# Kernel optimization log

Measured on AMD Instinct MI355X. Metric: run time of the kernel, lower is better.

## Reference

```python
import jax, jax.numpy as jnp
import numpy as np

B, GH, GW = 64, 14, 14
H = 512   # features_len == lstm hidden size == lstm_len
E = 512   # embedding_len
A = 512   # attention_len
V = 10000 # wordmap_len
MAXCAP = 50


def setup_inputs() -> dict:
    key = jax.random.key(0)
    ks = jax.random.split(key, 12)
    s = 0.02
    caplens = jax.random.randint(ks[2], (B, 1), 2, MAXCAP + 1, jnp.int32)
    caplens = caplens.at[0, 0].set(MAXCAP)  # ensure max(decode_lengths) == MAXCAP-1 (static T)
    return dict(
        image_features=jax.random.normal(ks[0], (B, GH, GW, H), jnp.float32),
        caps=jax.random.randint(ks[1], (B, MAXCAP), 0, V, jnp.int32),
        caplens=caplens,
        emb_table=jax.random.normal(ks[3], (V, E), jnp.float32) * s,
        W_ih=jax.random.normal(ks[4], (4 * H, E + H), jnp.float32) * s,
        W_hh=jax.random.normal(ks[5], (4 * H, H), jnp.float32) * s,
        b_ih=jnp.zeros((4 * H,), jnp.float32),
        b_hh=jnp.zeros((4 * H,), jnp.float32),
        W_enc=jax.random.normal(ks[6], (A, H), jnp.float32) * s,
        b_enc=jnp.zeros((A,), jnp.float32),
        W_dec=jax.random.normal(ks[7], (A, H), jnp.float32) * s,
        b_dec=jnp.zeros((A,), jnp.float32),
        W_full=jax.random.normal(ks[8], (1, A), jnp.float32) * s,
        b_full=jnp.zeros((1,), jnp.float32),
        W_score=jax.random.normal(ks[9], (V, H), jnp.float32) * s,
        b_score=jnp.zeros((V,), jnp.float32),
    )


def _forward(image_features, emb_table, W_ih, W_hh, b_ih, b_hh,
             W_enc, b_enc, W_dec, b_dec, W_full, b_full, W_score, b_score,
             caps, caplens):
    Bsz = image_features.shape[0]
    feats = image_features.reshape(Bsz, -1, image_features.shape[-1])  # (B, P, H)
    cl = caplens[:, 0]
    sort_ind = jnp.argsort(-cl)                      # descending sort by caption length
    cl = cl[sort_ind]
    feats = feats[sort_ind]
    caps_s = caps[sort_ind]
    decode_lengths = cl - 1
    T = caps.shape[1] - 1                            # static; setup guarantees max(decode_lengths)==T
    emb = emb_table[caps_s]                          # (B, MAXCAP, E)
    enc_att = jnp.einsum('bph,ah->bpa', feats, W_enc) + b_enc  # precomputed encoder attention proj
    mask = jnp.arange(T)[None, :] < decode_lengths[:, None]    # (B, T): row active at step t

    h0 = jnp.zeros((Bsz, feats.shape[-1]), feats.dtype)
    c0 = jnp.zeros_like(h0)

    def step(carry, xs):
        h, c = carry
        emb_t, m_t = xs                              # (B,E), (B,)
        # attention (show-attend-tell style)
        att2 = h @ W_dec.T + b_dec                   # (B, A)
        e = jnp.einsum('bpa,a->bp', jax.nn.relu(enc_att + att2[:, None, :]), W_full[0]) + b_full[0]
        alpha = jax.nn.softmax(e, axis=-1)           # (B, P)
        ctx = jnp.einsum('bp,bph->bh', alpha, feats) # (B, H)
        # LSTMCell
        x = jnp.concatenate([emb_t, ctx], axis=1)    # (B, E+H)
        gates = x @ W_ih.T + b_ih + h @ W_hh.T + b_hh
        i, f, g, o = jnp.split(gates, 4, axis=1)
        c_new = jax.nn.sigmoid(f) * c + jax.nn.sigmoid(i) * jnp.tanh(g)
        h_new = jax.nn.sigmoid(o) * jnp.tanh(c_new)
        score = h_new @ W_score.T + b_score          # (B, V)
        m = m_t[:, None]
        # rows past their decode length keep stale state and write zeros (matches :k slicing)
        h = jnp.where(m, h_new, h)
        c = jnp.where(m, c_new, c)
        return (h, c), (jnp.where(m, score, jnp.zeros((), score.dtype)),
                        jnp.where(m, alpha, jnp.zeros((), alpha.dtype)))

    (_, _), (scores, weights) = jax.lax.scan(
        step, (h0, c0), (emb[:, :T, :].transpose(1, 0, 2), mask.T))
    scores = scores.transpose(1, 0, 2)   # (B, T, V)
    weights = weights.transpose(1, 0, 2) # (B, T, P)
    return scores, caps_s, decode_lengths, weights, sort_ind


def reference(image_features, caps, caplens, emb_table, W_ih, W_hh, b_ih, b_hh,
              W_enc, b_enc, W_dec, b_dec, W_full, b_full, W_score, b_score):
    return _forward(image_features, emb_table, W_ih, W_hh, b_ih, b_hh,
                    W_enc, b_enc, W_dec, b_dec, W_full, b_full, W_score, b_score,
                    caps, caplens)
```

## Files before the change

### kernel.cpp

```cpp
#include <hip/hip_runtime.h>
#include <math.h>


#define WS_SORT   0
#define WS_DL     64
#define WS_NB     128
#define WS_ROWOFF 192
#define WS_CAPS   256
#define WS_RMAP   3456
#define WS_H      6592
#define WS_C      39360
#define WS_ATT2   72128
#define WS_E      104896
#define WS_Z      117696
#define WS_CTXP   117952
#define WS_PG     249024
#define WS_HALL   2346176
#define WS_ENC    3951808

#define OUT_SCORES 0
#define OUT_CAPS   31360000
#define OUT_DL     31363200
#define OUT_W      31363264
#define OUT_SORT   31977920

#define KC  32
#define LST 68

__device__ __forceinline__ float sigm(float x) { return 1.f / (1.f + expf(-x)); }

__device__ __forceinline__ void gemm_acc(const float* __restrict__ As, const float* __restrict__ Bs,
                                         float acc[8][8], int tx, int ty) {
#pragma unroll 8
  for (int kk = 0; kk < KC; ++kk) {
    const float4* ar = (const float4*)(As + kk * LST + tx * 8);
    const float4* br = (const float4*)(Bs + kk * LST + ty * 8);
    float4 a0 = ar[0], a1 = ar[1];
    float4 b0 = br[0], b1 = br[1];
    float av[8] = {a0.x, a0.y, a0.z, a0.w, a1.x, a1.y, a1.z, a1.w};
    float bv[8] = {b0.x, b0.y, b0.z, b0.w, b1.x, b1.y, b1.z, b1.w};
#pragma unroll
    for (int i = 0; i < 8; ++i)
#pragma unroll
      for (int j = 0; j < 8; ++j)
        acc[i][j] = fmaf(av[i], bv[j], acc[i][j]);
  }
}

__device__ __forceinline__ void load_tile_strided(const float* __restrict__ src, int row0, int ld, int k0,
                                                  float* __restrict__ dst, int tid, int nrows_valid) {
#pragma unroll
  for (int i = 0; i < 8; ++i) {
    int lin = tid + 64 * i;
    int m = lin >> 3, kf = lin & 7;
    float4 v = make_float4(0.f, 0.f, 0.f, 0.f);
    if (m < nrows_valid) v = *(const float4*)(src + (long)(row0 + m) * ld + k0 + kf * 4);
    dst[(kf * 4 + 0) * LST + m] = v.x;
    dst[(kf * 4 + 1) * LST + m] = v.y;
    dst[(kf * 4 + 2) * LST + m] = v.z;
    dst[(kf * 4 + 3) * LST + m] = v.w;
  }
}

__device__ __forceinline__ void load_tile_gather(const float* __restrict__ src, const int* __restrict__ bases,
                                                 int k0, float* __restrict__ dst, int tid) {
#pragma unroll
  for (int i = 0; i < 8; ++i) {
    int lin = tid + 64 * i;
    int m = lin >> 3, kf = lin & 7;
    float4 v = *(const float4*)(src + bases[m] + k0 + kf * 4);
    dst[(kf * 4 + 0) * LST + m] = v.x;
    dst[(kf * 4 + 1) * LST + m] = v.y;
    dst[(kf * 4 + 2) * LST + m] = v.z;
    dst[(kf * 4 + 3) * LST + m] = v.w;
  }
}

__global__ __launch_bounds__(64) void setup_kernel(const int* __restrict__ caps, const int* __restrict__ caplens,
                                                   float* __restrict__ ws, float* __restrict__ out) {
  __shared__ int cl_s[64], so_s[64], dl_s[64], nb_s[49], ro_s[50];
  int i = threadIdx.x;
  cl_s[i] = caplens[i];
  __syncthreads();
  int cli = cl_s[i];
  int r = 0;
  for (int j = 0; j < 64; ++j) {
    int clj = cl_s[j];
    r += (clj > cli) || (clj == cli && j < i);
  }
  so_s[r] = i;
  dl_s[r] = cli - 1;
  __syncthreads();
  int* iws = (int*)ws;
  iws[WS_SORT + i] = so_s[i];
  iws[WS_DL + i] = dl_s[i];
  out[OUT_SORT + i] = (float)so_s[i];
  out[OUT_DL + i] = (float)dl_s[i];
  if (i < 49) {
    int n = 0;
    for (int b = 0; b < 64; ++b) n += (dl_s[b] > i);
    iws[WS_NB + i] = n;
    nb_s[i] = n;
  }
  __syncthreads();
  if (i == 0) {
    int acc = 0;
    for (int t = 0; t < 49; ++t) { ro_s[t] = acc; acc += nb_s[t]; }
    ro_s[49] = acc;
    iws[WS_NB + 49] = acc;
  }
  __syncthreads();
  if (i < 50) iws[WS_ROWOFF + i] = ro_s[i];
  int R = ro_s[49];
  for (int rr = i; rr < 3136; rr += 64) {
    int val = 0;
    if (rr < R) {
      int t = 0;
      while (t < 48 && ro_s[t + 1] <= rr) ++t;
      val = t * 64 + (rr - ro_s[t]);
    }
    iws[WS_RMAP + rr] = val;
  }
  for (int j = i; j < 3200; j += 64) {
    int k = j / 50, jj = j - k * 50;
    int cv = caps[so_s[k] * 50 + jj];
    iws[WS_CAPS + j] = cv;
    out[OUT_CAPS + j] = (float)cv;
  }
}

__global__ void zero_init_kernel(float* __restrict__ out, float* __restrict__ ws, const float* __restrict__ b_dec) {
  const float4 z = make_float4(0.f, 0.f, 0.f, 0.f);
  float4* out4 = (float4*)out;
  float4* ws4 = (float4*)ws;
  const float4* bd4 = (const float4*)b_dec;
  for (long idx = (long)blockIdx.x * 256 + threadIdx.x; idx < 8018240L; idx += (long)gridDim.x * 256) {
    if (idx < 7840000L) {
      out4[idx] = z;
    } else if (idx < 7993664L) {
      out4[7840816L + (idx - 7840000L)] = z;
    } else if (idx < 8010048L) {
      ws4[1648L + (idx - 7993664L)] = z;
    } else {
      long j = idx - 8010048L;
      ws4[18032L + j] = bd4[j & 127];
    }
  }
}

__global__ __launch_bounds__(64) void encatt_kernel(const float* __restrict__ image, const float* __restrict__ W_enc,
                                                    const float* __restrict__ b_enc, float* __restrict__ ws) {
  __shared__ __align__(16) float As[KC * LST];
  __shared__ __align__(16) float Bs[KC * LST];
  __shared__ int rb[64];
  int tid = threadIdx.x;
  const int* iws = (const int*)ws;
  int mt = blockIdx.x, nt = blockIdx.y;
  {
    int r = mt * 64 + tid;
    int b = r / 196;
    int p = r - b * 196;
    rb[tid] = iws[WS_SORT + b] * 100352 + p * 512;
  }
  float acc[8][8] = {};
  for (int ch = 0; ch < 16; ++ch) {
    __syncthreads();
    load_tile_gather(image, rb, ch * 32, As, tid);
    load_tile_strided(W_enc, nt * 64, 512, ch * 32, Bs, tid, 64);
    __syncthreads();
    gemm_acc(As, Bs, acc, tid & 7, tid >> 3);
  }
  int tx = tid & 7, ty = tid >> 3;
  int r0 = mt * 64 + tx * 8;
  int n0 = nt * 64 + ty * 8;
#pragma unroll
  for (int i = 0; i < 8; ++i) {
    float* cp = ws + WS_ENC + (long)(r0 + i) * 512 + n0;
    *(float4*)(cp)     = make_float4(acc[i][0] + b_enc[n0],     acc[i][1] + b_enc[n0 + 1],
                                     acc[i][2] + b_enc[n0 + 2], acc[i][3] + b_enc[n0 + 3]);
    *(float4*)(cp + 4) = make_float4(acc[i][4] + b_enc[n0 + 4], acc[i][5] + b_enc[n0 + 5],
                                     acc[i][6] + b_enc[n0 + 6], acc[i][7] + b_enc[n0 + 7]);
  }
}

__global__ __launch_bounds__(256) void ectx_kernel(float* __restrict__ ws, const float* __restrict__ image,
                                                   const float* __restrict__ W_full, const float* __restrict__ b_full,
                                                   int t) {
  const int* iws = (const int*)ws;
  int b = blockIdx.x;
  if (b >= iws[WS_NB + t]) return;
  int pg = blockIdx.y;
  __shared__ float att2_s[512], wf_s[512], e_s[52];
  int tid = threadIdx.x;
  for (int a = tid; a < 512; a += 256) {
    att2_s[a] = ws[WS_ATT2 + b * 512 + a];
    wf_s[a] = W_full[a];
  }
  __syncthreads();
  int w = tid >> 6, lane = tid & 63;
  float bf0 = b_full[0];
  for (int idx = w; idx < 49; idx += 4) {
    int p = pg * 49 + idx;
    const float* er = ws + WS_ENC + (long)(b * 196 + p) * 512;
    float acc = 0.f;
#pragma unroll
    for (int a8 = 0; a8 < 8; ++a8) {
      int a = (a8 << 6) + lane;
      float v = er[a] + att2_s[a];
      acc = fmaf(fmaxf(v, 0.f), wf_s[a], acc);
    }
#pragma unroll
    for (int off = 32; off; off >>= 1) acc += __shfl_down(acc, off);
    if (lane == 0) e_s[idx] = expf(acc + bf0);
  }
  __syncthreads();
  if (tid < 49) ws[WS_E + b * 200 + pg * 49 + tid] = e_s[tid];
  if (tid == 0) {
    float zz = 0.f;
    for (int j = 0; j < 49; ++j) zz += e_s[j];
    ws[WS_Z + pg * 64 + b] = zz;
  }
  long sb = (long)iws[WS_SORT + b] * 100352;
  float a0 = 0.f, a1 = 0.f;
  for (int j = 0; j < 49; ++j) {
    float al = e_s[j];
    const float* fp = image + sb + (long)(pg * 49 + j) * 512;
    a0 = fmaf(al, fp[tid], a0);
    a1 = fmaf(al, fp[tid + 256], a1);
  }
  ws[WS_CTXP + pg * 32768 + b * 512 + tid] = a0;
  ws[WS_CTXP + pg * 32768 + b * 512 + 256 + tid] = a1;
}

__global__ __launch_bounds__(64) void gates_kernel(float* __restrict__ ws, const float* __restrict__ emb,
                                                   const float* __restrict__ W_ih, const float* __restrict__ W_hh,
                                                   int t) {
  __shared__ __align__(16) float As[KC * LST];
  __shared__ __align__(16) float Bs[KC * LST];
  __shared__ int rbe[64];
  __shared__ float rcpz_s[64];
  int tid = threadIdx.x;
  int nt = blockIdx.x;
  int ks = blockIdx.y;
  int* iws = (int*)ws;
  rbe[tid] = iws[WS_CAPS + tid * 50 + t] * 512;
  {
    float zz = ws[WS_Z + tid] + ws[WS_Z + 64 + tid] + ws[WS_Z + 128 + tid] + ws[WS_Z + 192 + tid];
    rcpz_s[tid] = 1.f / zz;
  }
  float acc[8][8] = {};
  for (int ch = 0; ch < 3; ++ch) {
    int k0 = ks * 96 + ch * 32;
    __syncthreads();
    if (k0 < 512) {
      load_tile_gather(emb, rbe, k0, As, tid);
    } else if (k0 < 1024) {
      int kc = k0 - 512;
#pragma unroll
      for (int i = 0; i < 8; ++i) {
        int lin = tid + 64 * i;
        int m = lin >> 3, kf = lin & 7;
        const float* base = ws + WS_CTXP + m * 512 + kc + kf * 4;
        float4 v0 = *(const float4*)(base);
        float4 v1 = *(const float4*)(base + 32768);
        float4 v2 = *(const float4*)(base + 65536);
        float4 v3 = *(const float4*)(base + 98304);
        float rz = rcpz_s[m];
        As[(kf * 4 + 0) * LST + m] = (v0.x + v1.x + v2.x + v3.x) * rz;
        As[(kf * 4 + 1) * LST + m] = (v0.y + v1.y + v2.y + v3.y) * rz;
        As[(kf * 4 + 2) * LST + m] = (v0.z + v1.z + v2.z + v3.z) * rz;
        As[(kf * 4 + 3) * LST + m] = (v0.w + v1.w + v2.w + v3.w) * rz;
      }
    } else {
      load_tile_strided(ws + WS_H, 0, 512, k0 - 1024, As, tid, 64);
    }
    if (k0 < 1024) load_tile_strided(W_ih, nt * 64, 1024, k0, Bs, tid, 64);
    else           load_tile_strided(W_hh, nt * 64, 512, k0 - 1024, Bs, tid, 64);
    __syncthreads();
    gemm_acc(As, Bs, acc, tid & 7, tid >> 3);
  }
  int tx = tid & 7, ty = tid >> 3;
  float* pg = ws + WS_PG + ks * 131072;
  int j0 = nt * 64 + ty * 8;
#pragma unroll
  for (int i = 0; i < 8; ++i) {
    int b = tx * 8 + i;
    float* cp = pg + b * 2048 + j0;
    *(float4*)(cp)     = make_float4(acc[i][0], acc[i][1], acc[i][2], acc[i][3]);
    *(float4*)(cp + 4) = make_float4(acc[i][4], acc[i][5], acc[i][6], acc[i][7]);
  }
}

__global__ __launch_bounds__(512) void lstm_att2_kernel(float* __restrict__ ws, const float* __restrict__ b_ih,
                                                        const float* __restrict__ b_hh, const float* __restrict__ W_dec,
                                                        const float* __restrict__ b_dec, float* __restrict__ out, int t) {
  const int* iws = (const int*)ws;
  int b = blockIdx.x;
  int as = blockIdx.y;
  int hh = threadIdx.x;
  int nb = iws[WS_NB + t];
  __shared__ float h_s[512], red[512];
  float gi = b_ih[hh] + b_hh[hh];
  float gf = b_ih[512 + hh] + b_hh[512 + hh];
  float gg = b_ih[1024 + hh] + b_hh[1024 + hh];
  float go = b_ih[1536 + hh] + b_hh[1536 + hh];
  const float* pgp = ws + WS_PG + b * 2048;
#pragma unroll
  for (int ks = 0; ks < 16; ++ks) {
    const float* p = pgp + ks * 131072;
    gi += p[hh]; gf += p[512 + hh]; gg += p[1024 + hh]; go += p[1536 + hh];
  }
  float c = ws[WS_C + b * 512 + hh];
  float cn = sigm(gf) * c + sigm(gi) * tanhf(gg);
  float hn = sigm(go) * tanhf(cn);
  h_s[hh] = hn;
  if (b < nb) {
    if (as == 0) {
      ws[WS_C + b * 512 + hh] = cn;
      ws[WS_H + b * 512 + hh] = hn;
      ws[WS_HALL + (long)(iws[WS_ROWOFF + t] + b) * 512 + hh] = hn;
    }
    if (hh < 49) {
      float zz = ws[WS_Z + b] + ws[WS_Z + 64 + b] + ws[WS_Z + 128 + b] + ws[WS_Z + 192 + b];
      int p = as * 49 + hh;
      out[OUT_W + (long)(b * 49 + t) * 196 + p] = ws[WS_E + b * 200 + p] / zz;
    }
  }
  __syncthreads();
  int a = as * 128 + (hh >> 2);
  int part = hh & 3;
  const float* wd = W_dec + (long)a * 512 + part * 128;
  const float* hp = h_s + part * 128;
  float s = 0.f;
#pragma unroll 8
  for (int j = 0; j < 32; ++j) {
    float4 wv = *(const float4*)(wd + 4 * j);
    s = fmaf(hp[4 * j], wv.x, s);
    s = fmaf(hp[4 * j + 1], wv.y, s);
    s = fmaf(hp[4 * j + 2], wv.z, s);
    s = fmaf(hp[4 * j + 3], wv.w, s);
  }
  red[hh] = s;
  __syncthreads();
  if (part == 0) {
    float v = red[hh] + red[hh + 1] + red[hh + 2] + red[hh + 3] + b_dec[a];
    ws[WS_ATT2 + b * 512 + a] = v;
  }
}

__global__ __launch_bounds__(64) void score_kernel(const float* __restrict__ ws, const float* __restrict__ W_score,
                                                   const float* __restrict__ b_score, float* __restrict__ out) {
  __shared__ __align__(16) float As[KC * LST];
  __shared__ __align__(16) float Bs[KC * LST];
  const int* iws = (const int*)ws;
  int mt = blockIdx.x, nt = blockIdx.y;
  int R = iws[WS_NB + 49];
  if (mt * 64 >= R) return;
  int tid = threadIdx.x;
  int mvalid = R - mt * 64; if (mvalid > 64) mvalid = 64;
  int nvalid = 10000 - nt * 64; if (nvalid > 64) nvalid = 64;
  float acc[8][8] = {};
  for (int ch = 0; ch < 16; ++ch) {
    __syncthreads();
    load_tile_strided(ws + WS_HALL, mt * 64, 512, ch * 32, As, tid, mvalid);
    load_tile_strided(W_score, nt * 64, 512, ch * 32, Bs, tid, nvalid);
    __syncthreads();
    gemm_acc(As, Bs, acc, tid & 7, tid >> 3);
  }
  int tx = tid & 7, ty = tid >> 3;
  int n0 = nt * 64 + ty * 8;
#pragma unroll
  for (int i = 0; i < 8; ++i) {
    int r = mt * 64 + tx * 8 + i;
    if (r >= R) continue;
    int tb = iws[WS_RMAP + r];
    int bb = tb & 63, tt = tb >> 6;
    float* cp = out + (long)bb * 490000 + tt * 10000 + n0;
    if (n0 + 4 <= 10000)
      *(float4*)(cp)     = make_float4(acc[i][0] + b_score[n0],     acc[i][1] + b_score[n0 + 1],
                                       acc[i][2] + b_score[n0 + 2], acc[i][3] + b_score[n0 + 3]);
    if (n0 + 8 <= 10000)
      *(float4*)(cp + 4) = make_float4(acc[i][4] + b_score[n0 + 4], acc[i][5] + b_score[n0 + 5],
                                       acc[i][6] + b_score[n0 + 6], acc[i][7] + b_score[n0 + 7]);
  }
}

extern "C" void kernel_launch(void* const* d_in, const int* in_sizes, int n_in,
                              void* d_out, int out_size, void* d_ws, size_t ws_size,
                              hipStream_t stream) {
  const float* image   = (const float*)d_in[0];
  const int*   caps    = (const int*)d_in[1];
  const int*   caplens = (const int*)d_in[2];
  const float* emb     = (const float*)d_in[3];
  const float* W_ih    = (const float*)d_in[4];
  const float* W_hh    = (const float*)d_in[5];
  const float* b_ih    = (const float*)d_in[6];
  const float* b_hh    = (const float*)d_in[7];
  const float* W_enc   = (const float*)d_in[8];
  const float* b_enc   = (const float*)d_in[9];
  const float* W_dec   = (const float*)d_in[10];
  const float* b_dec   = (const float*)d_in[11];
  const float* W_full  = (const float*)d_in[12];
  const float* b_full  = (const float*)d_in[13];
  const float* W_score = (const float*)d_in[14];
  const float* b_score = (const float*)d_in[15];
  float* out = (float*)d_out;
  float* ws  = (float*)d_ws;

  setup_kernel<<<1, 64, 0, stream>>>(caps, caplens, ws, out);
  zero_init_kernel<<<2048, 256, 0, stream>>>(out, ws, b_dec);
  encatt_kernel<<<dim3(196, 8), 64, 0, stream>>>(image, W_enc, b_enc, ws);
  for (int t = 0; t < 49; ++t) {
    ectx_kernel<<<dim3(64, 4), 256, 0, stream>>>(ws, image, W_full, b_full, t);
    gates_kernel<<<dim3(32, 16), 64, 0, stream>>>(ws, emb, W_ih, W_hh, t);
    lstm_att2_kernel<<<dim3(64, 4), 512, 0, stream>>>(ws, b_ih, b_hh, W_dec, b_dec, out, t);
  }
  score_kernel<<<dim3(49, 157), 64, 0, stream>>>(ws, W_score, b_score, out);
}
```

Baseline: 2.873 ms.

## Fuse per-step decoder kernels into one persistent kernel with grid barriers

Replaces the 147 per-timestep launches (ectx, gates, lstm_att2) with a single persistent 256-block kernel that loops over all 49 steps and separates phases with an atomic-counter grid barrier. The gates GEMM is remapped so each 256-thread block runs two 64x64 tiles, splitting K across wave pairs and reducing them through shared memory. The LSTM/att2 phase now uses 256 threads with float4 partial-gate sums. This targets launch overhead and inter-kernel gaps, but relies on all 256 blocks being co-resident to avoid deadlock and adds spin-wait barrier latency.

```diff
diff --git a/kernel.cpp b/kernel.cpp
--- a/kernel.cpp
+++ b/kernel.cpp
@@ -17,6 +17,7 @@
 #define WS_PG     249024
 #define WS_HALL   2346176
 #define WS_ENC    3951808
+#define WS_BAR    (WS_NB + 60)
 
 #define OUT_SCORES 0
 #define OUT_CAPS   31360000
@@ -28,6 +29,10 @@
 #define LST 68
 
 __device__ __forceinline__ float sigm(float x) { return 1.f / (1.f + expf(-x)); }
+
+__device__ __forceinline__ float4 f4add(float4 a, float4 b) {
+  return make_float4(a.x + b.x, a.y + b.y, a.z + b.z, a.w + b.w);
+}
 
 __device__ __forceinline__ void gemm_acc(const float* __restrict__ As, const float* __restrict__ Bs,
                                          float acc[8][8], int tx, int ty) {
@@ -76,6 +81,17 @@
   }
 }
 
+__device__ __forceinline__ void gsync(int* bar, int target) {
+  __syncthreads();
+  if (threadIdx.x == 0) {
+    __hip_atomic_fetch_add(bar, 1, __ATOMIC_RELEASE, __HIP_MEMORY_SCOPE_AGENT);
+    while (__hip_atomic_load(bar, __ATOMIC_RELAXED, __HIP_MEMORY_SCOPE_AGENT) < target)
+      __builtin_amdgcn_s_sleep(1);
+    __threadfence();
+  }
+  __syncthreads();
+}
+
 __global__ __launch_bounds__(64) void setup_kernel(const int* __restrict__ caps, const int* __restrict__ caplens,
                                                    float* __restrict__ ws, float* __restrict__ out) {
   __shared__ int cl_s[64], so_s[64], dl_s[64], nb_s[49], ro_s[50];
@@ -92,6 +108,7 @@
   dl_s[r] = cli - 1;
   __syncthreads();
   int* iws = (int*)ws;
+  if (i == 0) iws[WS_BAR] = 0;
   iws[WS_SORT + i] = so_s[i];
   iws[WS_DL + i] = dl_s[i];
   out[OUT_SORT + i] = (float)so_s[i];
@@ -183,168 +200,222 @@
   }
 }
 
-__global__ __launch_bounds__(256) void ectx_kernel(float* __restrict__ ws, const float* __restrict__ image,
-                                                   const float* __restrict__ W_full, const float* __restrict__ b_full,
-                                                   int t) {
+__global__ __launch_bounds__(256) void loop_kernel(
+    float* __restrict__ ws, const float* __restrict__ image, const float* __restrict__ emb,
+    const float* __restrict__ W_ih, const float* __restrict__ W_hh,
+    const float* __restrict__ b_ih, const float* __restrict__ b_hh,
+    const float* __restrict__ W_dec, const float* __restrict__ b_dec,
+    const float* __restrict__ W_full, const float* __restrict__ b_full,
+    float* __restrict__ out) {
+  __shared__ __align__(16) float sm[8704];
+  int* bar = ((int*)ws) + WS_BAR;
   const int* iws = (const int*)ws;
-  int b = blockIdx.x;
-  if (b >= iws[WS_NB + t]) return;
-  int pg = blockIdx.y;
-  __shared__ float att2_s[512], wf_s[512], e_s[52];
+  int blk = blockIdx.x;
   int tid = threadIdx.x;
-  for (int a = tid; a < 512; a += 256) {
-    att2_s[a] = ws[WS_ATT2 + b * 512 + a];
-    wf_s[a] = W_full[a];
-  }
-  __syncthreads();
-  int w = tid >> 6, lane = tid & 63;
-  float bf0 = b_full[0];
-  for (int idx = w; idx < 49; idx += 4) {
-    int p = pg * 49 + idx;
-    const float* er = ws + WS_ENC + (long)(b * 196 + p) * 512;
-    float acc = 0.f;
-#pragma unroll
-    for (int a8 = 0; a8 < 8; ++a8) {
-      int a = (a8 << 6) + lane;
-      float v = er[a] + att2_s[a];
-      acc = fmaf(fmaxf(v, 0.f), wf_s[a], acc);
+  int syncno = 0;
+
+  for (int t = 0; t < 49; ++t) {
+    int nbt = iws[WS_NB + t];
+
+    {
+      int b = blk >> 2, pg = blk & 3;
+      if (b < nbt) {
+        float* att2_s = sm;
+        float* wf_s = sm + 512;
+        float* e_s = sm + 1024;
+        for (int a = tid; a < 512; a += 256) {
+          att2_s[a] = ws[WS_ATT2 + b * 512 + a];
+          wf_s[a] = W_full[a];
+        }
+        __syncthreads();
+        int w = tid >> 6, lane = tid & 63;
+        float bf0 = b_full[0];
+        for (int idx = w; idx < 49; idx += 4) {
+          int p = pg * 49 + idx;
+          const float* er = ws + WS_ENC + (long)(b * 196 + p) * 512;
+          float acc = 0.f;
+#pragma unroll
+          for (int a8 = 0; a8 < 8; ++a8) {
+            int a = (a8 << 6) + lane;
+            float v = er[a] + att2_s[a];
+            acc = fmaf(fmaxf(v, 0.f), wf_s[a], acc);
+          }
+#pragma unroll
+          for (int off = 32; off; off >>= 1) acc += __shfl_down(acc, off);
+          if (lane == 0) e_s[idx] = expf(acc + bf0);
+        }
+        __syncthreads();
+        if (tid < 49) ws[WS_E + b * 200 + pg * 49 + tid] = e_s[tid];
+        if (tid == 0) {
+          float zz = 0.f;
+          for (int j = 0; j < 49; ++j) zz += e_s[j];
+          ws[WS_Z + pg * 64 + b] = zz;
+        }
+        long sb = (long)iws[WS_SORT + b] * 100352;
+        float a0 = 0.f, a1 = 0.f;
+        for (int j = 0; j < 49; ++j) {
+          float al = e_s[j];
+          const float* fp = image + sb + (long)(pg * 49 + j) * 512;
+          a0 = fmaf(al, fp[tid], a0);
+          a1 = fmaf(al, fp[tid + 256], a1);
+        }
+        ws[WS_CTXP + pg * 32768 + b * 512 + tid] = a0;
+        ws[WS_CTXP + pg * 32768 + b * 512 + 256 + tid] = a1;
+      }
     }
-#pragma unroll
-    for (int off = 32; off; off >>= 1) acc += __shfl_down(acc, off);
-    if (lane == 0) e_s[idx] = expf(acc + bf0);
-  }
-  __syncthreads();
-  if (tid < 49) ws[WS_E + b * 200 + pg * 49 + tid] = e_s[tid];
-  if (tid == 0) {
-    float zz = 0.f;
-    for (int j = 0; j < 49; ++j) zz += e_s[j];
-    ws[WS_Z + pg * 64 + b] = zz;
-  }
-  long sb = (long)iws[WS_SORT + b] * 100352;
-  float a0 = 0.f, a1 = 0.f;
-  for (int j = 0; j < 49; ++j) {
-    float al = e_s[j];
-    const float* fp = image + sb + (long)(pg * 49 + j) * 512;
-    a0 = fmaf(al, fp[tid], a0);
-    a1 = fmaf(al, fp[tid + 256], a1);
-  }
-  ws[WS_CTXP + pg * 32768 + b * 512 + tid] = a0;
-  ws[WS_CTXP + pg * 32768 + b * 512 + 256 + tid] = a1;
-}
-
-__global__ __launch_bounds__(64) void gates_kernel(float* __restrict__ ws, const float* __restrict__ emb,
-                                                   const float* __restrict__ W_ih, const float* __restrict__ W_hh,
-                                                   int t) {
-  __shared__ __align__(16) float As[KC * LST];
-  __shared__ __align__(16) float Bs[KC * LST];
-  __shared__ int rbe[64];
-  __shared__ float rcpz_s[64];
-  int tid = threadIdx.x;
-  int nt = blockIdx.x;
-  int ks = blockIdx.y;
-  int* iws = (int*)ws;
-  rbe[tid] = iws[WS_CAPS + tid * 50 + t] * 512;
-  {
-    float zz = ws[WS_Z + tid] + ws[WS_Z + 64 + tid] + ws[WS_Z + 128 + tid] + ws[WS_Z + 192 + tid];
-    rcpz_s[tid] = 1.f / zz;
-  }
-  float acc[8][8] = {};
-  for (int ch = 0; ch < 3; ++ch) {
-    int k0 = ks * 96 + ch * 32;
-    __syncthreads();
-    if (k0 < 512) {
-      load_tile_gather(emb, rbe, k0, As, tid);
-    } else if (k0 < 1024) {
-      int kc = k0 - 512;
-#pragma unroll
-      for (int i = 0; i < 8; ++i) {
-        int lin = tid + 64 * i;
-        int m = lin >> 3, kf = lin & 7;
-        const float* base = ws + WS_CTXP + m * 512 + kc + kf * 4;
-        float4 v0 = *(const float4*)(base);
-        float4 v1 = *(const float4*)(base + 32768);
-        float4 v2 = *(const float4*)(base + 65536);
-        float4 v3 = *(const float4*)(base + 98304);
-        float rz = rcpz_s[m];
-        As[(kf * 4 + 0) * LST + m] = (v0.x + v1.x + v2.x + v3.x) * rz;
-        As[(kf * 4 + 1) * LST + m] = (v0.y + v1.y + v2.y + v3.y) * rz;
-        As[(kf * 4 + 2) * LST + m] = (v0.z + v1.z + v2.z + v3.z) * rz;
-        As[(kf * 4 + 3) * LST + m] = (v0.w + v1.w + v2.w + v3.w) * rz;
-      }
-    } else {
-      load_tile_strided(ws + WS_H, 0, 512, k0 - 1024, As, tid, 64);
+    ++syncno; gsync(bar, 256 * syncno);
+
+    {
+      int w = tid >> 6, lane = tid & 63;
+      int pairIdx = w >> 1, sub = w & 1;
+      int vb = blk * 2 + pairIdx;
+      int nt = vb & 31, ks = vb >> 5;
+      float* As_w = sm + w * 1088;
+      float* Bs_w = sm + 4352 + w * 1088;
+      int tx = lane & 7, ty = lane >> 3;
+      float acc[8][8] = {};
+      for (int c = 0; c < 3; ++c) {
+        int k0 = ks * 96 + (sub * 3 + c) * 16;
+#pragma unroll
+        for (int i = 0; i < 4; ++i) {
+          int lin = lane + 64 * i;
+          int m = lin >> 2, kf = lin & 3;
+          float4 v;
+          if (k0 < 512) {
+            v = *(const float4*)(emb + (long)iws[WS_CAPS + m * 50 + t] * 512 + k0 + kf * 4);
+          } else if (k0 < 1024) {
+            const float* base = ws + WS_CTXP + m * 512 + (k0 - 512) + kf * 4;
+            float4 v0 = *(const float4*)(base);
+            float4 v1 = *(const float4*)(base + 32768);
+            float4 v2 = *(const float4*)(base + 65536);
+            float4 v3 = *(const float4*)(base + 98304);
+            float rz = 1.f / (ws[WS_Z + m] + ws[WS_Z + 64 + m] + ws[WS_Z + 128 + m] + ws[WS_Z + 192 + m]);
+            v = make_float4((v0.x + v1.x + v2.x + v3.x) * rz, (v0.y + v1.y + v2.y + v3.y) * rz,
+                            (v0.z + v1.z + v2.z + v3.z) * rz, (v0.w + v1.w + v2.w + v3.w) * rz);
+          } else {
+            v = *(const float4*)(ws + WS_H + m * 512 + (k0 - 1024) + kf * 4);
+          }
+          As_w[(kf * 4 + 0) * 68 + m] = v.x;
+          As_w[(kf * 4 + 1) * 68 + m] = v.y;
+          As_w[(kf * 4 + 2) * 68 + m] = v.z;
+          As_w[(kf * 4 + 3) * 68 + m] = v.w;
+        }
+#pragma unroll
+        for (int i = 0; i < 4; ++i) {
+          int lin = lane + 64 * i;
+          int m = lin >> 2, kf = lin & 3;
+          const float* src = (k0 < 1024) ? (W_ih + (long)(nt * 64 + m) * 1024 + k0 + kf * 4)
+                                         : (W_hh + (long)(nt * 64 + m) * 512 + (k0 - 1024) + kf * 4);
+          float4 v = *(const float4*)src;
+          Bs_w[(kf * 4 + 0) * 68 + m] = v.x;
+          Bs_w[(kf * 4 + 1) * 68 + m] = v.y;
+          Bs_w[(kf * 4 + 2) * 68 + m] = v.z;
+          Bs_w[(kf * 4 + 3) * 68 + m] = v.w;
+        }
+        __syncthreads();
+#pragma unroll
+        for (int kk = 0; kk < 16; ++kk) {
+          const float4* ar4 = (const float4*)(As_w + kk * 68 + tx * 8);
+          const float4* br4 = (const float4*)(Bs_w + kk * 68 + ty * 8);
+          float4 a0v = ar4[0], a1v = ar4[1];
+          float4 b0v = br4[0], b1v = br4[1];
+          float av[8] = {a0v.x, a0v.y, a0v.z, a0v.w, a1v.x, a1v.y, a1v.z, a1v.w};
+          float bv[8] = {b0v.x, b0v.y, b0v.z, b0v.w, b1v.x, b1v.y, b1v.z, b1v.w};
+#pragma unroll
+          for (int i = 0; i < 8; ++i)
+#pragma unroll
+            for (int j = 0; j < 8; ++j)
+              acc[i][j] = fmaf(av[i], bv[j], acc[i][j]);
+        }
+        __syncthreads();
+      }
+      float* ar = sm + pairIdx * 4096;
+      if (sub == 0) {
+#pragma unroll
+        for (int i = 0; i < 8; ++i) {
+          float* dp = ar + (tx * 8 + i) * 64 + ty * 8;
+          *(float4*)(dp)     = make_float4(acc[i][0], acc[i][1], acc[i][2], acc[i][3]);
+          *(float4*)(dp + 4) = make_float4(acc[i][4], acc[i][5], acc[i][6], acc[i][7]);
+        }
+      }
+      __syncthreads();
+      if (sub == 1) {
+        float* pgout = ws + WS_PG + ks * 131072;
+#pragma unroll
+        for (int i = 0; i < 8; ++i) {
+          const float* sp = ar + (tx * 8 + i) * 64 + ty * 8;
+          float4 r0 = *(const float4*)(sp);
+          float4 r1 = *(const float4*)(sp + 4);
+          float* cp = pgout + (tx * 8 + i) * 2048 + nt * 64 + ty * 8;
+          *(float4*)(cp)     = make_float4(acc[i][0] + r0.x, acc[i][1] + r0.y,
+                                           acc[i][2] + r0.z, acc[i][3] + r0.w);
+          *(float4*)(cp + 4) = make_float4(acc[i][4] + r1.x, acc[i][5] + r1.y,
+                                           acc[i][6] + r1.z, acc[i][7] + r1.w);
+        }
+      }
     }
-    if (k0 < 1024) load_tile_strided(W_ih, nt * 64, 1024, k0, Bs, tid, 64);
-    else           load_tile_strided(W_hh, nt * 64, 512, k0 - 1024, Bs, tid, 64);
-    __syncthreads();
-    gemm_acc(As, Bs, acc, tid & 7, tid >> 3);
-  }
-  int tx = tid & 7, ty = tid >> 3;
-  float* pg = ws + WS_PG + ks * 131072;
-  int j0 = nt * 64 + ty * 8;
-#pragma unroll
-  for (int i = 0; i < 8; ++i) {
-    int b = tx * 8 + i;
-    float* cp = pg + b * 2048 + j0;
-    *(float4*)(cp)     = make_float4(acc[i][0], acc[i][1], acc[i][2], acc[i][3]);
-    *(float4*)(cp + 4) = make_float4(acc[i][4], acc[i][5], acc[i][6], acc[i][7]);
-  }
-}
-
-__global__ __launch_bounds__(512) void lstm_att2_kernel(float* __restrict__ ws, const float* __restrict__ b_ih,
-                                                        const float* __restrict__ b_hh, const float* __restrict__ W_dec,
-                                                        const float* __restrict__ b_dec, float* __restrict__ out, int t) {
-  const int* iws = (const int*)ws;
-  int b = blockIdx.x;
-  int as = blockIdx.y;
-  int hh = threadIdx.x;
-  int nb = iws[WS_NB + t];
-  __shared__ float h_s[512], red[512];
-  float gi = b_ih[hh] + b_hh[hh];
-  float gf = b_ih[512 + hh] + b_hh[512 + hh];
-  float gg = b_ih[1024 + hh] + b_hh[1024 + hh];
-  float go = b_ih[1536 + hh] + b_hh[1536 + hh];
-  const float* pgp = ws + WS_PG + b * 2048;
-#pragma unroll
-  for (int ks = 0; ks < 16; ++ks) {
-    const float* p = pgp + ks * 131072;
-    gi += p[hh]; gf += p[512 + hh]; gg += p[1024 + hh]; go += p[1536 + hh];
-  }
-  float c = ws[WS_C + b * 512 + hh];
-  float cn = sigm(gf) * c + sigm(gi) * tanhf(gg);
-  float hn = sigm(go) * tanhf(cn);
-  h_s[hh] = hn;
-  if (b < nb) {
-    if (as == 0) {
-      ws[WS_C + b * 512 + hh] = cn;
-      ws[WS_H + b * 512 + hh] = hn;
-      ws[WS_HALL + (long)(iws[WS_ROWOFF + t] + b) * 512 + hh] = hn;
+    ++syncno; gsync(bar, 256 * syncno);
+
+    {
+      int b = blk >> 2, as = blk & 3;
+      bool act = (b < nbt);
+      float* g = sm;
+      float* hsh = sm + 2048;
+      float* red = sm + 2560;
+      const float4* bi4 = (const float4*)b_ih;
+      const float4* bh4 = (const float4*)b_hh;
+      const float* pgb = ws + WS_PG + b * 2048;
+      int f0 = tid, f1 = tid + 256;
+      float4 A0 = f4add(bi4[f0], bh4[f0]);
+      float4 A1 = f4add(bi4[f1], bh4[f1]);
+#pragma unroll
+      for (int ksl = 0; ksl < 16; ++ksl) {
+        const float4* p = (const float4*)(pgb + ksl * 131072);
+        A0 = f4add(A0, p[f0]);
+        A1 = f4add(A1, p[f1]);
+      }
+      ((float4*)g)[f0] = A0;
+      ((float4*)g)[f1] = A1;
+      __syncthreads();
+      int ro = iws[WS_ROWOFF + t];
+#pragma unroll
+      for (int r = 0; r < 2; ++r) {
+        int hh = tid + r * 256;
+        float gi = g[hh], gf = g[512 + hh], gg = g[1024 + hh], go = g[1536 + hh];
+        float c = ws[WS_C + b * 512 + hh];
+        float cn = sigm(gf) * c + sigm(gi) * tanhf(gg);
+        float hn = sigm(go) * tanhf(cn);
+        hsh[hh] = hn;
+        if (act && as == 0) {
+          ws[WS_C + b * 512 + hh] = cn;
+          ws[WS_H + b * 512 + hh] = hn;
+          ws[WS_HALL + (long)(ro + b) * 512 + hh] = hn;
+        }
+      }
+      if (act && tid < 49) {
+        float zz = ws[WS_Z + b] + ws[WS_Z + 64 + b] + ws[WS_Z + 128 + b] + ws[WS_Z + 192 + b];
+        int p = as * 49 + tid;
+        out[OUT_W + (long)(b * 49 + t) * 196 + p] = ws[WS_E + b * 200 + p] / zz;
+      }
+      __syncthreads();
+      int a = as * 128 + (tid >> 1);
+      int part = tid & 1;
+      const float4* wd = (const float4*)(W_dec + (long)a * 512 + part * 256);
+      const float4* hp = (const float4*)(hsh + part * 256);
+      float s = 0.f;
+#pragma unroll 8
+      for (int j = 0; j < 64; ++j) {
+        float4 wv = wd[j], hv = hp[j];
+        s = fmaf(wv.x, hv.x, s);
+        s = fmaf(wv.y, hv.y, s);
+        s = fmaf(wv.z, hv.z, s);
+        s = fmaf(wv.w, hv.w, s);
+      }
+      red[tid] = s;
+      __syncthreads();
+      if (part == 0) ws[WS_ATT2 + b * 512 + a] = red[tid] + red[tid + 1] + b_dec[a];
     }
-    if (hh < 49) {
-      float zz = ws[WS_Z + b] + ws[WS_Z + 64 + b] + ws[WS_Z + 128 + b] + ws[WS_Z + 192 + b];
-      int p = as * 49 + hh;
-      out[OUT_W + (long)(b * 49 + t) * 196 + p] = ws[WS_E + b * 200 + p] / zz;
-    }
-  }
-  __syncthreads();
-  int a = as * 128 + (hh >> 2);
-  int part = hh & 3;
-  const float* wd = W_dec + (long)a * 512 + part * 128;
-  const float* hp = h_s + part * 128;
-  float s = 0.f;
-#pragma unroll 8
-  for (int j = 0; j < 32; ++j) {
-    float4 wv = *(const float4*)(wd + 4 * j);
-    s = fmaf(hp[4 * j], wv.x, s);
-    s = fmaf(hp[4 * j + 1], wv.y, s);
-    s = fmaf(hp[4 * j + 2], wv.z, s);
-    s = fmaf(hp[4 * j + 3], wv.w, s);
-  }
-  red[hh] = s;
-  __syncthreads();
-  if (part == 0) {
-    float v = red[hh] + red[hh + 1] + red[hh + 2] + red[hh + 3] + b_dec[a];
-    ws[WS_ATT2 + b * 512 + a] = v;
+    if (t < 48) { ++syncno; gsync(bar, 256 * syncno); }
   }
 }
 
@@ -410,10 +481,7 @@
   setup_kernel<<<1, 64, 0, stream>>>(caps, caplens, ws, out);
   zero_init_kernel<<<2048, 256, 0, stream>>>(out, ws, b_dec);
   encatt_kernel<<<dim3(196, 8), 64, 0, stream>>>(image, W_enc, b_enc, ws);
-  for (int t = 0; t < 49; ++t) {
-    ectx_kernel<<<dim3(64, 4), 256, 0, stream>>>(ws, image, W_full, b_full, t);
-    gates_kernel<<<dim3(32, 16), 64, 0, stream>>>(ws, emb, W_ih, W_hh, t);
-    lstm_att2_kernel<<<dim3(64, 4), 512, 0, stream>>>(ws, b_ih, b_hh, W_dec, b_dec, out, t);
-  }
+  loop_kernel<<<256, 256, 0, stream>>>(ws, image, emb, W_ih, W_hh, b_ih, b_hh,
+                                       W_dec, b_dec, W_full, b_full, out);
   score_kernel<<<dim3(49, 157), 64, 0, stream>>>(ws, W_score, b_score, out);
 }
```

After: 9.591 ms. 3.34x slower.

## Fuse LSTM cell, decoder attention and context into one per-step kernel; enlarge GEMM tiles

Applied to the files above, without the earlier changes.

Merges the per-step attention/context kernel and the LSTM/att2 kernel into a single step_kernel run by one block per batch row. That block computes the LSTM update, att2, attention softmax and the normalized context for the next step. This cuts the per-step launch count from three to two and removes the partial-sum scratch buffers and the reduction inside the gates kernel. In exchange, only 64 blocks do all 196 pixels of attention per step, which reduces parallelism. The encoder-attention and score GEMMs also move to 128x128 tiles with 256 threads.

```diff
diff --git a/kernel.cpp b/kernel.cpp
--- a/kernel.cpp
+++ b/kernel.cpp
@@ -10,13 +10,10 @@
 #define WS_RMAP   3456
 #define WS_H      6592
 #define WS_C      39360
-#define WS_ATT2   72128
-#define WS_E      104896
-#define WS_Z      117696
-#define WS_CTXP   117952
-#define WS_PG     249024
-#define WS_HALL   2346176
-#define WS_ENC    3951808
+#define WS_CTX    72128
+#define WS_PG     104896
+#define WS_HALL   2202048
+#define WS_ENC    3807680
 
 #define OUT_SCORES 0
 #define OUT_CAPS   31360000
@@ -26,8 +23,13 @@
 
 #define KC  32
 #define LST 68
+#define LKW 132
 
 __device__ __forceinline__ float sigm(float x) { return 1.f / (1.f + expf(-x)); }
+
+__device__ __forceinline__ float4 f4add(float4 a, float4 b) {
+  return make_float4(a.x + b.x, a.y + b.y, a.z + b.z, a.w + b.w);
+}
 
 __device__ __forceinline__ void gemm_acc(const float* __restrict__ As, const float* __restrict__ Bs,
                                          float acc[8][8], int tx, int ty) {
@@ -76,6 +78,53 @@
   }
 }
 
+__device__ __forceinline__ void stage128_strided(const float* __restrict__ src, int row0, int ld, int k0,
+                                                 float* __restrict__ dst, int tid, int nrows_valid) {
+#pragma unroll
+  for (int i = 0; i < 2; ++i) {
+    int lin = tid + 256 * i;
+    int m = lin >> 2, kf = lin & 3;
+    float4 v = make_float4(0.f, 0.f, 0.f, 0.f);
+    if (m < nrows_valid) v = *(const float4*)(src + (long)(row0 + m) * ld + k0 + kf * 4);
+    dst[(kf * 4 + 0) * LKW + m] = v.x;
+    dst[(kf * 4 + 1) * LKW + m] = v.y;
+    dst[(kf * 4 + 2) * LKW + m] = v.z;
+    dst[(kf * 4 + 3) * LKW + m] = v.w;
+  }
+}
+
+__device__ __forceinline__ void stage128_gather(const float* __restrict__ src, const int* __restrict__ bases,
+                                                int k0, float* __restrict__ dst, int tid) {
+#pragma unroll
+  for (int i = 0; i < 2; ++i) {
+    int lin = tid + 256 * i;
+    int m = lin >> 2, kf = lin & 3;
+    float4 v = *(const float4*)(src + bases[m] + k0 + kf * 4);
+    dst[(kf * 4 + 0) * LKW + m] = v.x;
+    dst[(kf * 4 + 1) * LKW + m] = v.y;
+    dst[(kf * 4 + 2) * LKW + m] = v.z;
+    dst[(kf * 4 + 3) * LKW + m] = v.w;
+  }
+}
+
+__device__ __forceinline__ void gemm_acc128(const float* __restrict__ As, const float* __restrict__ Bs,
+                                            float acc[8][8], int tx, int ty) {
+#pragma unroll
+  for (int kk = 0; kk < 16; ++kk) {
+    const float4* ar = (const float4*)(As + kk * LKW + tx * 8);
+    const float4* br = (const float4*)(Bs + kk * LKW + ty * 8);
+    float4 a0 = ar[0], a1 = ar[1];
+    float4 b0 = br[0], b1 = br[1];
+    float av[8] = {a0.x, a0.y, a0.z, a0.w, a1.x, a1.y, a1.z, a1.w};
+    float bv[8] = {b0.x, b0.y, b0.z, b0.w, b1.x, b1.y, b1.z, b1.w};
+#pragma unroll
+    for (int i = 0; i < 8; ++i)
+#pragma unroll
+      for (int j = 0; j < 8; ++j)
+        acc[i][j] = fmaf(av[i], bv[j], acc[i][j]);
+  }
+}
+
 __global__ __launch_bounds__(64) void setup_kernel(const int* __restrict__ caps, const int* __restrict__ caplens,
                                                    float* __restrict__ ws, float* __restrict__ out) {
   __shared__ int cl_s[64], so_s[64], dl_s[64], nb_s[49], ro_s[50];
@@ -129,50 +178,46 @@
   }
 }
 
-__global__ void zero_init_kernel(float* __restrict__ out, float* __restrict__ ws, const float* __restrict__ b_dec) {
+__global__ void zero_init_kernel(float* __restrict__ out, float* __restrict__ ws) {
   const float4 z = make_float4(0.f, 0.f, 0.f, 0.f);
   float4* out4 = (float4*)out;
   float4* ws4 = (float4*)ws;
-  const float4* bd4 = (const float4*)b_dec;
-  for (long idx = (long)blockIdx.x * 256 + threadIdx.x; idx < 8018240L; idx += (long)gridDim.x * 256) {
+  for (long idx = (long)blockIdx.x * 256 + threadIdx.x; idx < 8010048L; idx += (long)gridDim.x * 256) {
     if (idx < 7840000L) {
       out4[idx] = z;
     } else if (idx < 7993664L) {
       out4[7840816L + (idx - 7840000L)] = z;
-    } else if (idx < 8010048L) {
+    } else {
       ws4[1648L + (idx - 7993664L)] = z;
-    } else {
-      long j = idx - 8010048L;
-      ws4[18032L + j] = bd4[j & 127];
-    }
-  }
-}
-
-__global__ __launch_bounds__(64) void encatt_kernel(const float* __restrict__ image, const float* __restrict__ W_enc,
-                                                    const float* __restrict__ b_enc, float* __restrict__ ws) {
-  __shared__ __align__(16) float As[KC * LST];
-  __shared__ __align__(16) float Bs[KC * LST];
-  __shared__ int rb[64];
+    }
+  }
+}
+
+__global__ __launch_bounds__(256) void encatt_kernel(const float* __restrict__ image, const float* __restrict__ W_enc,
+                                                     const float* __restrict__ b_enc, float* __restrict__ ws) {
+  __shared__ __align__(16) float As[16 * LKW];
+  __shared__ __align__(16) float Bs[16 * LKW];
+  __shared__ int rb[128];
   int tid = threadIdx.x;
   const int* iws = (const int*)ws;
   int mt = blockIdx.x, nt = blockIdx.y;
-  {
-    int r = mt * 64 + tid;
+  if (tid < 128) {
+    int r = mt * 128 + tid;
     int b = r / 196;
     int p = r - b * 196;
     rb[tid] = iws[WS_SORT + b] * 100352 + p * 512;
   }
   float acc[8][8] = {};
-  for (int ch = 0; ch < 16; ++ch) {
-    __syncthreads();
-    load_tile_gather(image, rb, ch * 32, As, tid);
-    load_tile_strided(W_enc, nt * 64, 512, ch * 32, Bs, tid, 64);
-    __syncthreads();
-    gemm_acc(As, Bs, acc, tid & 7, tid >> 3);
-  }
-  int tx = tid & 7, ty = tid >> 3;
-  int r0 = mt * 64 + tx * 8;
-  int n0 = nt * 64 + ty * 8;
+  for (int ch = 0; ch < 32; ++ch) {
+    __syncthreads();
+    stage128_gather(image, rb, ch * 16, As, tid);
+    stage128_strided(W_enc, nt * 128, 512, ch * 16, Bs, tid, 128);
+    __syncthreads();
+    gemm_acc128(As, Bs, acc, tid & 15, tid >> 4);
+  }
+  int tx = tid & 15, ty = tid >> 4;
+  int r0 = mt * 128 + tx * 8;
+  int n0 = nt * 128 + ty * 8;
 #pragma unroll
   for (int i = 0; i < 8; ++i) {
     float* cp = ws + WS_ENC + (long)(r0 + i) * 512 + n0;
@@ -183,71 +228,17 @@
   }
 }
 
-__global__ __launch_bounds__(256) void ectx_kernel(float* __restrict__ ws, const float* __restrict__ image,
-                                                   const float* __restrict__ W_full, const float* __restrict__ b_full,
-                                                   int t) {
-  const int* iws = (const int*)ws;
-  int b = blockIdx.x;
-  if (b >= iws[WS_NB + t]) return;
-  int pg = blockIdx.y;
-  __shared__ float att2_s[512], wf_s[512], e_s[52];
-  int tid = threadIdx.x;
-  for (int a = tid; a < 512; a += 256) {
-    att2_s[a] = ws[WS_ATT2 + b * 512 + a];
-    wf_s[a] = W_full[a];
-  }
-  __syncthreads();
-  int w = tid >> 6, lane = tid & 63;
-  float bf0 = b_full[0];
-  for (int idx = w; idx < 49; idx += 4) {
-    int p = pg * 49 + idx;
-    const float* er = ws + WS_ENC + (long)(b * 196 + p) * 512;
-    float acc = 0.f;
-#pragma unroll
-    for (int a8 = 0; a8 < 8; ++a8) {
-      int a = (a8 << 6) + lane;
-      float v = er[a] + att2_s[a];
-      acc = fmaf(fmaxf(v, 0.f), wf_s[a], acc);
-    }
-#pragma unroll
-    for (int off = 32; off; off >>= 1) acc += __shfl_down(acc, off);
-    if (lane == 0) e_s[idx] = expf(acc + bf0);
-  }
-  __syncthreads();
-  if (tid < 49) ws[WS_E + b * 200 + pg * 49 + tid] = e_s[tid];
-  if (tid == 0) {
-    float zz = 0.f;
-    for (int j = 0; j < 49; ++j) zz += e_s[j];
-    ws[WS_Z + pg * 64 + b] = zz;
-  }
-  long sb = (long)iws[WS_SORT + b] * 100352;
-  float a0 = 0.f, a1 = 0.f;
-  for (int j = 0; j < 49; ++j) {
-    float al = e_s[j];
-    const float* fp = image + sb + (long)(pg * 49 + j) * 512;
-    a0 = fmaf(al, fp[tid], a0);
-    a1 = fmaf(al, fp[tid + 256], a1);
-  }
-  ws[WS_CTXP + pg * 32768 + b * 512 + tid] = a0;
-  ws[WS_CTXP + pg * 32768 + b * 512 + 256 + tid] = a1;
-}
-
 __global__ __launch_bounds__(64) void gates_kernel(float* __restrict__ ws, const float* __restrict__ emb,
                                                    const float* __restrict__ W_ih, const float* __restrict__ W_hh,
                                                    int t) {
   __shared__ __align__(16) float As[KC * LST];
   __shared__ __align__(16) float Bs[KC * LST];
   __shared__ int rbe[64];
-  __shared__ float rcpz_s[64];
   int tid = threadIdx.x;
   int nt = blockIdx.x;
   int ks = blockIdx.y;
   int* iws = (int*)ws;
   rbe[tid] = iws[WS_CAPS + tid * 50 + t] * 512;
-  {
-    float zz = ws[WS_Z + tid] + ws[WS_Z + 64 + tid] + ws[WS_Z + 128 + tid] + ws[WS_Z + 192 + tid];
-    rcpz_s[tid] = 1.f / zz;
-  }
   float acc[8][8] = {};
   for (int ch = 0; ch < 3; ++ch) {
     int k0 = ks * 96 + ch * 32;
@@ -255,22 +246,7 @@
     if (k0 < 512) {
       load_tile_gather(emb, rbe, k0, As, tid);
     } else if (k0 < 1024) {
-      int kc = k0 - 512;
-#pragma unroll
-      for (int i = 0; i < 8; ++i) {
-        int lin = tid + 64 * i;
-        int m = lin >> 3, kf = lin & 7;
-        const float* base = ws + WS_CTXP + m * 512 + kc + kf * 4;
-        float4 v0 = *(const float4*)(base);
-        float4 v1 = *(const float4*)(base + 32768);
-        float4 v2 = *(const float4*)(base + 65536);
-        float4 v3 = *(const float4*)(base + 98304);
-        float rz = rcpz_s[m];
-        As[(kf * 4 + 0) * LST + m] = (v0.x + v1.x + v2.x + v3.x) * rz;
-        As[(kf * 4 + 1) * LST + m] = (v0.y + v1.y + v2.y + v3.y) * rz;
-        As[(kf * 4 + 2) * LST + m] = (v0.z + v1.z + v2.z + v3.z) * rz;
-        As[(kf * 4 + 3) * LST + m] = (v0.w + v1.w + v2.w + v3.w) * rz;
-      }
+      load_tile_strided(ws + WS_CTX, 0, 512, k0 - 512, As, tid, 64);
     } else {
       load_tile_strided(ws + WS_H, 0, 512, k0 - 1024, As, tid, 64);
     }
@@ -291,87 +267,143 @@
   }
 }
 
-__global__ __launch_bounds__(512) void lstm_att2_kernel(float* __restrict__ ws, const float* __restrict__ b_ih,
-                                                        const float* __restrict__ b_hh, const float* __restrict__ W_dec,
-                                                        const float* __restrict__ b_dec, float* __restrict__ out, int t) {
+__global__ __launch_bounds__(256) void step_kernel(float* __restrict__ ws, const float* __restrict__ image,
+                                                   const float* __restrict__ b_ih, const float* __restrict__ b_hh,
+                                                   const float* __restrict__ W_dec, const float* __restrict__ b_dec,
+                                                   const float* __restrict__ W_full, const float* __restrict__ b_full,
+                                                   float* __restrict__ out, int t) {
+  __shared__ float g[2048];
+  __shared__ float h_s[512], att2_s[512], wf_s[512], e_s[200], ctxp_s[2048], zsh[4];
   const int* iws = (const int*)ws;
-  int b = blockIdx.x;
-  int as = blockIdx.y;
-  int hh = threadIdx.x;
-  int nb = iws[WS_NB + t];
-  __shared__ float h_s[512], red[512];
-  float gi = b_ih[hh] + b_hh[hh];
-  float gf = b_ih[512 + hh] + b_hh[512 + hh];
-  float gg = b_ih[1024 + hh] + b_hh[1024 + hh];
-  float go = b_ih[1536 + hh] + b_hh[1536 + hh];
-  const float* pgp = ws + WS_PG + b * 2048;
-#pragma unroll
-  for (int ks = 0; ks < 16; ++ks) {
-    const float* p = pgp + ks * 131072;
-    gi += p[hh]; gf += p[512 + hh]; gg += p[1024 + hh]; go += p[1536 + hh];
-  }
-  float c = ws[WS_C + b * 512 + hh];
-  float cn = sigm(gf) * c + sigm(gi) * tanhf(gg);
-  float hn = sigm(go) * tanhf(cn);
-  h_s[hh] = hn;
-  if (b < nb) {
-    if (as == 0) {
-      ws[WS_C + b * 512 + hh] = cn;
-      ws[WS_H + b * 512 + hh] = hn;
-      ws[WS_HALL + (long)(iws[WS_ROWOFF + t] + b) * 512 + hh] = hn;
-    }
-    if (hh < 49) {
-      float zz = ws[WS_Z + b] + ws[WS_Z + 64 + b] + ws[WS_Z + 128 + b] + ws[WS_Z + 192 + b];
-      int p = as * 49 + hh;
-      out[OUT_W + (long)(b * 49 + t) * 196 + p] = ws[WS_E + b * 200 + p] / zz;
-    }
-  }
-  __syncthreads();
-  int a = as * 128 + (hh >> 2);
-  int part = hh & 3;
-  const float* wd = W_dec + (long)a * 512 + part * 128;
-  const float* hp = h_s + part * 128;
-  float s = 0.f;
-#pragma unroll 8
-  for (int j = 0; j < 32; ++j) {
-    float4 wv = *(const float4*)(wd + 4 * j);
-    s = fmaf(hp[4 * j], wv.x, s);
-    s = fmaf(hp[4 * j + 1], wv.y, s);
-    s = fmaf(hp[4 * j + 2], wv.z, s);
-    s = fmaf(hp[4 * j + 3], wv.w, s);
-  }
-  red[hh] = s;
-  __syncthreads();
-  if (part == 0) {
-    float v = red[hh] + red[hh + 1] + red[hh + 2] + red[hh + 3] + b_dec[a];
-    ws[WS_ATT2 + b * 512 + a] = v;
-  }
-}
-
-__global__ __launch_bounds__(64) void score_kernel(const float* __restrict__ ws, const float* __restrict__ W_score,
-                                                   const float* __restrict__ b_score, float* __restrict__ out) {
-  __shared__ __align__(16) float As[KC * LST];
-  __shared__ __align__(16) float Bs[KC * LST];
+  int b = blockIdx.x, tid = threadIdx.x;
+  int tw = t + 1;
+
+  if (t >= 0) {
+    const float4* bi4 = (const float4*)b_ih;
+    const float4* bh4 = (const float4*)b_hh;
+    int f0 = tid, f1 = tid + 256;
+    float4 A0 = f4add(bi4[f0], bh4[f0]);
+    float4 A1 = f4add(bi4[f1], bh4[f1]);
+    const float* pgb = ws + WS_PG + b * 2048;
+#pragma unroll
+    for (int ks = 0; ks < 16; ++ks) {
+      const float4* p = (const float4*)(pgb + (long)ks * 131072);
+      A0 = f4add(A0, p[f0]);
+      A1 = f4add(A1, p[f1]);
+    }
+    ((float4*)g)[f0] = A0;
+    ((float4*)g)[f1] = A1;
+    __syncthreads();
+    bool act = b < iws[WS_NB + t];
+    int ro = iws[WS_ROWOFF + t];
+#pragma unroll
+    for (int r = 0; r < 2; ++r) {
+      int hh = tid + 256 * r;
+      float gi = g[hh], gf = g[512 + hh], gg = g[1024 + hh], go = g[1536 + hh];
+      float c = ws[WS_C + b * 512 + hh];
+      float cn = sigm(gf) * c + sigm(gi) * tanhf(gg);
+      float hn = sigm(go) * tanhf(cn);
+      h_s[hh] = hn;
+      if (act) {
+        ws[WS_C + b * 512 + hh] = cn;
+        ws[WS_H + b * 512 + hh] = hn;
+        ws[WS_HALL + (long)(ro + b) * 512 + hh] = hn;
+      }
+    }
+    if (tw > 48 || b >= iws[WS_NB + tw]) return;
+    __syncthreads();
+    const float4* h4 = (const float4*)h_s;
+#pragma unroll
+    for (int it = 0; it < 2; ++it) {
+      int a = it * 256 + tid;
+      const float4* wd = (const float4*)(W_dec + (long)a * 512);
+      float s = 0.f;
+#pragma unroll 16
+      for (int j = 0; j < 128; ++j) {
+        float4 wv = wd[j], hv = h4[j];
+        s = fmaf(wv.x, hv.x, s);
+        s = fmaf(wv.y, hv.y, s);
+        s = fmaf(wv.z, hv.z, s);
+        s = fmaf(wv.w, hv.w, s);
+      }
+      att2_s[a] = s + b_dec[a];
+    }
+  } else {
+    att2_s[tid] = b_dec[tid];
+    att2_s[tid + 256] = b_dec[tid + 256];
+  }
+
+  for (int a = tid; a < 512; a += 256) wf_s[a] = W_full[a];
+  __syncthreads();
+
+  int w = tid >> 6, lane = tid & 63;
+  float bf0 = b_full[0];
+  for (int idx = w; idx < 196; idx += 4) {
+    const float* er = ws + WS_ENC + (long)(b * 196 + idx) * 512;
+    float acc = 0.f;
+#pragma unroll
+    for (int a8 = 0; a8 < 8; ++a8) {
+      int a = (a8 << 6) + lane;
+      float v = er[a] + att2_s[a];
+      acc = fmaf(fmaxf(v, 0.f), wf_s[a], acc);
+    }
+#pragma unroll
+    for (int off = 32; off; off >>= 1) acc += __shfl_down(acc, off);
+    if (lane == 0) e_s[idx] = expf(acc + bf0);
+  }
+  __syncthreads();
+  float zv = (tid < 196) ? e_s[tid] : 0.f;
+#pragma unroll
+  for (int off = 32; off; off >>= 1) zv += __shfl_down(zv, off);
+  if (lane == 0) zsh[w] = zv;
+  __syncthreads();
+  float rz = 1.f / (zsh[0] + zsh[1] + zsh[2] + zsh[3]);
+  bool wr = (t >= 0) || (b < iws[WS_NB + 0]);
+  if (wr && tid < 196) out[OUT_W + (long)(b * 49 + tw) * 196 + tid] = e_s[tid] * rz;
+  long sb = (long)iws[WS_SORT + b] * 100352;
+  float ac[8] = {};
+  for (int j = 0; j < 49; ++j) {
+    int p = w * 49 + j;
+    float al = e_s[p];
+    const float* fp = image + sb + (long)p * 512;
+#pragma unroll
+    for (int jj = 0; jj < 8; ++jj) ac[jj] = fmaf(al, fp[lane + 64 * jj], ac[jj]);
+  }
+#pragma unroll
+  for (int jj = 0; jj < 8; ++jj) ctxp_s[w * 512 + lane + 64 * jj] = ac[jj];
+  __syncthreads();
+#pragma unroll
+  for (int r = 0; r < 2; ++r) {
+    int d = tid + 256 * r;
+    ws[WS_CTX + b * 512 + d] =
+        (ctxp_s[d] + ctxp_s[512 + d] + ctxp_s[1024 + d] + ctxp_s[1536 + d]) * rz;
+  }
+}
+
+__global__ __launch_bounds__(256) void score_kernel(const float* __restrict__ ws, const float* __restrict__ W_score,
+                                                    const float* __restrict__ b_score, float* __restrict__ out) {
+  __shared__ __align__(16) float As[16 * LKW];
+  __shared__ __align__(16) float Bs[16 * LKW];
   const int* iws = (const int*)ws;
   int mt = blockIdx.x, nt = blockIdx.y;
   int R = iws[WS_NB + 49];
-  if (mt * 64 >= R) return;
+  if (mt * 128 >= R) return;
   int tid = threadIdx.x;
-  int mvalid = R - mt * 64; if (mvalid > 64) mvalid = 64;
-  int nvalid = 10000 - nt * 64; if (nvalid > 64) nvalid = 64;
+  int mvalid = R - mt * 128; if (mvalid > 128) mvalid = 128;
+  int nvalid = 10000 - nt * 128; if (nvalid > 128) nvalid = 128;
   float acc[8][8] = {};
-  for (int ch = 0; ch < 16; ++ch) {
-    __syncthreads();
-    load_tile_strided(ws + WS_HALL, mt * 64, 512, ch * 32, As, tid, mvalid);
-    load_tile_strided(W_score, nt * 64, 512, ch * 32, Bs, tid, nvalid);
-    __syncthreads();
-    gemm_acc(As, Bs, acc, tid & 7, tid >> 3);
-  }
-  int tx = tid & 7, ty = tid >> 3;
-  int n0 = nt * 64 + ty * 8;
+  for (int ch = 0; ch < 32; ++ch) {
+    __syncthreads();
+    stage128_strided(ws + WS_HALL, mt * 128, 512, ch * 16, As, tid, mvalid);
+    stage128_strided(W_score, nt * 128, 512, ch * 16, Bs, tid, nvalid);
+    __syncthreads();
+    gemm_acc128(As, Bs, acc, tid & 15, tid >> 4);
+  }
+  int tx = tid & 15, ty = tid >> 4;
+  int n0 = nt * 128 + ty * 8;
 #pragma unroll
   for (int i = 0; i < 8; ++i) {
-    int r = mt * 64 + tx * 8 + i;
+    int r = mt * 128 + tx * 8 + i;
     if (r >= R) continue;
     int tb = iws[WS_RMAP + r];
     int bb = tb & 63, tt = tb >> 6;
@@ -408,12 +440,12 @@
   float* ws  = (float*)d_ws;
 
   setup_kernel<<<1, 64, 0, stream>>>(caps, caplens, ws, out);
-  zero_init_kernel<<<2048, 256, 0, stream>>>(out, ws, b_dec);
-  encatt_kernel<<<dim3(196, 8), 64, 0, stream>>>(image, W_enc, b_enc, ws);
+  zero_init_kernel<<<2048, 256, 0, stream>>>(out, ws);
+  encatt_kernel<<<dim3(98, 4), 256, 0, stream>>>(image, W_enc, b_enc, ws);
+  step_kernel<<<64, 256, 0, stream>>>(ws, image, b_ih, b_hh, W_dec, b_dec, W_full, b_full, out, -1);
   for (int t = 0; t < 49; ++t) {
-    ectx_kernel<<<dim3(64, 4), 256, 0, stream>>>(ws, image, W_full, b_full, t);
     gates_kernel<<<dim3(32, 16), 64, 0, stream>>>(ws, emb, W_ih, W_hh, t);
-    lstm_att2_kernel<<<dim3(64, 4), 512, 0, stream>>>(ws, b_ih, b_hh, W_dec, b_dec, out, t);
-  }
-  score_kernel<<<dim3(49, 157), 64, 0, stream>>>(ws, W_score, b_score, out);
-}
+    step_kernel<<<64, 256, 0, stream>>>(ws, image, b_ih, b_hh, W_dec, b_dec, W_full, b_full, out, t);
+  }
+  score_kernel<<<dim3(25, 79), 256, 0, stream>>>(ws, W_score, b_score, out);
+}
```

Result: slower. 5.633 ms (+96.1%).
